# Optimization experiments

Measured on AMD Instinct MI355X. Metric: run time of the kernel, lower is better.

Reference implementation:

```python
import jax, jax.numpy as jnp
import numpy as np

LOG_2PI = np.float32(np.log(2.0 * np.pi))


def _expect(features, labels, pi, mu, sigma):
    # features [N,A], labels [N], pi [C,K], mu [C,K,A], sigma [C,K,A,A]
    d = features.shape[1]
    K = pi.shape[1]
    pi_n = pi[labels]                      # [N,K]
    mu_n = mu[labels]                      # [N,K,A]
    # invert / slogdet per (class, cluster) once, then gather (same math as
    # inverting the per-sample gathered sigma, but C*K inversions not N*K)
    inv_sigma = jnp.linalg.inv(sigma)[labels]          # [N,K,A,A]
    logdet = jnp.linalg.slogdet(sigma)[1][labels]      # [N,K]
    diff = features[:, None, :] - mu_n                 # [N,K,A]
    dist = jnp.einsum('nkd,nkde,nke->nk', diff, inv_sigma, diff)
    # NOTE: sign of the d*log(2pi) term follows the original code verbatim
    log_p = -(dist - d * LOG_2PI + logdet) / 2.0       # [N,K]
    onehot = jax.nn.one_hot(jnp.argmax(log_p, axis=1), K, dtype=features.dtype)
    q_un = onehot * pi_n
    return q_un / (q_un.sum(axis=1, keepdims=True) + 1e-30)


def setup_inputs() -> dict:
    key = jax.random.key(0)
    ks = jax.random.split(key, 6)
    N, C, K, A = 2048, 100, 4, 128
    features = jax.random.normal(ks[0], (N, A), dtype=jnp.float32)
    weight = jax.random.normal(ks[1], (C, A), dtype=jnp.float32) * 0.05
    bias = jnp.zeros((C,), dtype=jnp.float32)
    pi = jax.random.uniform(ks[2], (C, K), dtype=jnp.float32) + 0.1
    pi = pi / pi.sum(axis=1, keepdims=True)
    mu = jax.random.normal(ks[3], (C, K, A), dtype=jnp.float32)
    # SPD covariance stack: B B^T / A + I
    B = jax.random.normal(ks[4], (C, K, A, A), dtype=jnp.float32) * 0.3
    sigma = jnp.einsum('ckij,cklj->ckil', B, B) / A + jnp.eye(A, dtype=jnp.float32)
    labels = jax.random.randint(ks[5], (N,), 0, C, dtype=jnp.int64)
    ratio = jnp.float32(0.5)
    return {"features": features, "weight": weight, "bias": bias,
            "pi": pi, "mu": mu, "sigma": sigma, "labels": labels,
            "ratio": ratio}


def reference(features, weight, bias, pi, mu, sigma, labels, ratio):
    N, A = features.shape
    C, K = pi.shape
    y = features @ weight.T + bias                     # fc(features)  [N,C]
    # NxW_ij - NxW_kj : row j of W minus row label[n] of W, per sample
    diff_w = weight[None, :, :] - weight[labels][:, None, :]   # [N,C,A]
    q = _expect(features, labels, pi, mu, sigma)               # [N,K]
    onehot_q = jax.nn.one_hot(jnp.argmax(q, axis=1), K, dtype=features.dtype)
    CV = jnp.einsum('nkde,nk->nde', sigma[labels], onehot_q)   # [N,A,A]
    # diagonal of ratio * (dW) CV (dW)^T, computed without the [N,C,C] matrix
    sigma2 = ratio * jnp.einsum('nca,nab,ncb->nc', diff_w, CV, diff_w)
    aug = y + 0.5 * sigma2                                     # [N,C]
    logp = jax.nn.log_softmax(aug, axis=-1)
    loss = -jnp.mean(jnp.take_along_axis(logp, labels[:, None], axis=1))
    return (loss, y)
```

## Files before the change

### kernel.cpp

```cpp
#include <hip/hip_runtime.h>
#include <hip/hip_bf16.h>
#include <cmath>

#define N_S    2048
#define C_CLS  100
#define K_CL   4
#define A_DIM  128
#define LDSROW 132
#define NB     16
#define MAXPER 96
#define WTPAD  101
#define SPB    8

__device__ __forceinline__ float gj_invert_lds(
    float* As, float* Rbuf, float* DinvS, int tid)
{
    const int lane = tid & 63;
    const int wv   = tid >> 6;
    float logdet = 0.0f;

    for (int t = 0; t < 8; ++t) {
        const int p0 = NB * t;

        if (wv == 0) {
            const int r = lane >> 2, cg = lane & 3;
            float4 dv = *(const float4*)&As[(p0 + r) * LDSROW + p0 + 4 * cg];
            #pragma unroll
            for (int p = 0; p < NB; ++p) {
                const int sel = p & 3, pr4 = p >> 2;
                float te = (sel == 0) ? dv.x : (sel == 1) ? dv.y : (sel == 2) ? dv.z : dv.w;
                float piv = __shfl(te, (p << 2) | pr4, 64);
                float ip  = 1.0f / piv;
                logdet += __logf(piv);
                const int rowsrc = (p << 2) | cg;
                float4 prs;
                prs.x = __shfl(dv.x, rowsrc, 64) * ip;
                prs.y = __shfl(dv.y, rowsrc, 64) * ip;
                prs.z = __shfl(dv.z, rowsrc, 64) * ip;
                prs.w = __shfl(dv.w, rowsrc, 64) * ip;
                if (cg == pr4) (&prs.x)[sel] = ip;
                float f = __shfl(te, (lane & ~3) | pr4, 64);
                if (r == p) {
                    dv = prs;
                } else {
                    dv.x -= f * prs.x; dv.y -= f * prs.y;
                    dv.z -= f * prs.z; dv.w -= f * prs.w;
                    if (cg == pr4) (&dv.x)[sel] = -f * ip;
                }
            }
            DinvS[r * 17 + 4 * cg + 0] = dv.x;
            DinvS[r * 17 + 4 * cg + 1] = dv.y;
            DinvS[r * 17 + 4 * cg + 2] = dv.z;
            DinvS[r * 17 + 4 * cg + 3] = dv.w;
        }
        __syncthreads();

        {
            const int rr = tid >> 5, j4c = tid & 31;
            float4 o;
            if ((j4c >> 2) == t) {
                const int cg = j4c & 3;
                o.x = DinvS[rr * 17 + 4 * cg + 0];
                o.y = DinvS[rr * 17 + 4 * cg + 1];
                o.z = DinvS[rr * 17 + 4 * cg + 2];
                o.w = DinvS[rr * 17 + 4 * cg + 3];
            } else {
                o.x = 0.f; o.y = 0.f; o.z = 0.f; o.w = 0.f;
                #pragma unroll 4
                for (int k = 0; k < NB; ++k) {
                    const float a = DinvS[rr * 17 + k];
                    const float4 s4 = *(const float4*)&As[(p0 + k) * LDSROW + 4 * j4c];
                    o.x += a * s4.x; o.y += a * s4.y; o.z += a * s4.z; o.w += a * s4.w;
                }
            }
            *(float4*)&Rbuf[rr * A_DIM + 4 * j4c] = o;
        }
        __syncthreads();

        if (tid < 448) {
            const int rgi = tid >> 4;
            const int cp  = tid & 15;
            const int rga = (rgi < 4 * t) ? rgi : rgi + 4;
            const int row0 = 4 * rga;
            const int c0 = 8 * cp, c1 = 8 * cp + 4;
            const bool pcol = ((cp >> 1) == t);
            float4 a00, a01, a10, a11, a20, a21, a30, a31;
            if (pcol) {
                a00 = a01 = a10 = a11 = a20 = a21 = a30 = a31 = (float4){0, 0, 0, 0};
            } else {
                a00 = *(const float4*)&As[(row0 + 0) * LDSROW + c0];
                a01 = *(const float4*)&As[(row0 + 0) * LDSROW + c1];
                a10 = *(const float4*)&As[(row0 + 1) * LDSROW + c0];
                a11 = *(const float4*)&As[(row0 + 1) * LDSROW + c1];
                a20 = *(const float4*)&As[(row0 + 2) * LDSROW + c0];
                a21 = *(const float4*)&As[(row0 + 2) * LDSROW + c1];
                a30 = *(const float4*)&As[(row0 + 3) * LDSROW + c0];
                a31 = *(const float4*)&As[(row0 + 3) * LDSROW + c1];
            }
            #pragma unroll 4
            for (int k = 0; k < NB; ++k) {
                const float4 r0 = *(const float4*)&Rbuf[k * A_DIM + c0];
                const float4 r1 = *(const float4*)&Rbuf[k * A_DIM + c1];
                const float f0 = As[(row0 + 0) * LDSROW + p0 + k];
                const float f1 = As[(row0 + 1) * LDSROW + p0 + k];
                const float f2 = As[(row0 + 2) * LDSROW + p0 + k];
                const float f3 = As[(row0 + 3) * LDSROW + p0 + k];
                a00.x -= f0 * r0.x; a00.y -= f0 * r0.y; a00.z -= f0 * r0.z; a00.w -= f0 * r0.w;
                a01.x -= f0 * r1.x; a01.y -= f0 * r1.y; a01.z -= f0 * r1.z; a01.w -= f0 * r1.w;
                a10.x -= f1 * r0.x; a10.y -= f1 * r0.y; a10.z -= f1 * r0.z; a10.w -= f1 * r0.w;
                a11.x -= f1 * r1.x; a11.y -= f1 * r1.y; a11.z -= f1 * r1.z; a11.w -= f1 * r1.w;
                a20.x -= f2 * r0.x; a20.y -= f2 * r0.y; a20.z -= f2 * r0.z; a20.w -= f2 * r0.w;
                a21.x -= f2 * r1.x; a21.y -= f2 * r1.y; a21.z -= f2 * r1.z; a21.w -= f2 * r1.w;
                a30.x -= f3 * r0.x; a30.y -= f3 * r0.y; a30.z -= f3 * r0.z; a30.w -= f3 * r0.w;
                a31.x -= f3 * r1.x; a31.y -= f3 * r1.y; a31.z -= f3 * r1.z; a31.w -= f3 * r1.w;
            }
            *(float4*)&As[(row0 + 0) * LDSROW + c0] = a00;
            *(float4*)&As[(row0 + 0) * LDSROW + c1] = a01;
            *(float4*)&As[(row0 + 1) * LDSROW + c0] = a10;
            *(float4*)&As[(row0 + 1) * LDSROW + c1] = a11;
            *(float4*)&As[(row0 + 2) * LDSROW + c0] = a20;
            *(float4*)&As[(row0 + 2) * LDSROW + c1] = a21;
            *(float4*)&As[(row0 + 3) * LDSROW + c0] = a30;
            *(float4*)&As[(row0 + 3) * LDSROW + c1] = a31;
        }
        {
            const int rr = tid >> 5, j4c = tid & 31;
            *(float4*)&As[(p0 + rr) * LDSROW + 4 * j4c] =
                *(const float4*)&Rbuf[rr * A_DIM + 4 * j4c];
        }
        __syncthreads();
    }
    return logdet;
}

template<int R>
__device__ __forceinline__ void gsweep(
    const float* __restrict__ As, const float* __restrict__ weight,
    int c0, int lane, float wc0, float wc1, int bid,
    float* __restrict__ gdiag, float* __restrict__ gcol)
{
    const int c0u = __builtin_amdgcn_readfirstlane(c0);
    const float* wr[R];
    #pragma unroll
    for (int r = 0; r < R; ++r) {
        int c = c0u + r; c = (c < C_CLS) ? c : (C_CLS - 1);
        wr[r] = weight + (size_t)c * A_DIM;
    }
    float h0[R], h1[R];
    #pragma unroll
    for (int r = 0; r < R; ++r) { h0[r] = 0.f; h1[r] = 0.f; }
    #pragma unroll 2
    for (int i = 0; i < A_DIM; ++i) {
        const float s0 = As[i * LDSROW + lane];
        const float s1 = As[i * LDSROW + 64 + lane];
        #pragma unroll
        for (int r = 0; r < R; ++r) {
            const float b = wr[r][i];
            h0[r] += b * s0; h1[r] += b * s1;
        }
    }
    #pragma unroll
    for (int r = 0; r < R; ++r) {
        const int c = c0 + r;
        if (c < C_CLS) {
            float pd = h0[r] * weight[c * A_DIM + lane]
                     + h1[r] * weight[c * A_DIM + 64 + lane];
            float pc = h0[r] * wc0 + h1[r] * wc1;
            #pragma unroll
            for (int off = 32; off; off >>= 1) {
                pd += __shfl_xor(pd, off, 64);
                pc += __shfl_xor(pc, off, 64);
            }
            if (lane == 0) {
                gdiag[bid * C_CLS + c] = pd;
                gcol [bid * C_CLS + c] = pc;
            }
        }
    }
}

__global__ __launch_bounds__(512, 2) void k_fused(
    const float* __restrict__ sigma, const float* __restrict__ mu,
    const float* __restrict__ features, const int* __restrict__ labels,
    const float* __restrict__ weight, float* __restrict__ score,
    float* __restrict__ gdiag, float* __restrict__ gcol)
{
    __shared__ __align__(16) float As[A_DIM * LDSROW];
    __shared__ __align__(16) float Scratch[NB * A_DIM + 16*33];
    __shared__ float DinvS[NB * 17];
    __shared__ float ldS;
    __shared__ int idxL[MAXPER];
    __shared__ int cntA;

    const int tid  = threadIdx.x;
    const int bid  = blockIdx.x;
    const int cl   = bid >> 2;
    const int lane = tid & 63;
    const int wv   = tid >> 6;

    if (tid == 0) cntA = 0;

    const float4* src = (const float4*)(sigma + (size_t)bid * A_DIM * A_DIM);
    for (int e4 = tid; e4 < A_DIM * 32; e4 += 512) {
        int i = e4 >> 5, j4 = e4 & 31;
        *(float4*)&As[i * LDSROW + 4 * j4] = src[e4];
    }
    __syncthreads();

    for (int n = tid; n < N_S; n += 512) {
        if (labels[n] == cl) {
            int s = atomicAdd(&cntA, 1);
            if (s < MAXPER) idxL[s] = n;
        }
    }
    {
        const float wc0 = weight[cl * A_DIM + lane];
        const float wc1 = weight[cl * A_DIM + 64 + lane];
        gsweep<13>(As, weight, wv * 13, lane, wc0, wc1, bid, gdiag, gcol);
    }
    __syncthreads();

    float logdet = gj_invert_lds(As, Scratch, DinvS, tid);
    if (tid == 0) ldS = logdet;
    __syncthreads();
    const float ld = ldS;
    const int cnt = min(cntA, MAXPER);

    float* Dbuf = Scratch;
    float* Par  = Scratch + NB * A_DIM;
    const int s16 = tid >> 5;
    const int fc  = tid & 31;
    const float4 muv = ((const float4*)mu)[bid * 32 + fc];

    for (int c0 = 0; c0 < cnt; c0 += 16) {
        const int m = cnt - c0 < 16 ? cnt - c0 : 16;
        if (s16 < m) {
            const int n = idxL[c0 + s16];
            const float4 f = ((const float4*)features)[n * 32 + fc];
            float4 dv;
            dv.x = f.x - muv.x; dv.y = f.y - muv.y;
            dv.z = f.z - muv.z; dv.w = f.w - muv.w;
            *(float4*)&Dbuf[s16 * A_DIM + 4 * fc] = dv;
        }
        __syncthreads();
        if (s16 < m) {
            float4 p = {0.f, 0.f, 0.f, 0.f};
            #pragma unroll 4
            for (int i = 0; i < A_DIM; ++i) {
                const float  d = Dbuf[s16 * A_DIM + i];
                const float4 a = *(const float4*)&As[i * LDSROW + 4 * fc];
                p.x += d * a.x; p.y += d * a.y; p.z += d * a.z; p.w += d * a.w;
            }
            const float4 dj = *(const float4*)&Dbuf[s16 * A_DIM + 4 * fc];
            Par[s16 * 33 + fc] = p.x * dj.x + p.y * dj.y + p.z * dj.z + p.w * dj.w;
        }
        __syncthreads();
        if (tid < m) {
            const int n = idxL[c0 + tid];
            float q = 0.f;
            #pragma unroll
            for (int j = 0; j < 32; ++j) q += Par[tid * 33 + j];
            score[n * K_CL + (bid & 3)] = q + ld;
        }
        __syncthreads();
    }
}

__global__ __launch_bounds__(256) void k_out(
    const float* __restrict__ features, const float* __restrict__ weight,
    const float* __restrict__ bias, const int* __restrict__ labels,
    const float* __restrict__ score, const float* __restrict__ gdiag,
    const float* __restrict__ gcol, const float* __restrict__ ratio_p,
    float* __restrict__ y, float* __restrict__ loss)
{
    __shared__ float Wt[A_DIM * WTPAD];
    __shared__ float bs[C_CLS];
    __shared__ __align__(16) float xs[2][A_DIM];
    __shared__ float red[2][2], red2[2][2], acl_s[2], lsum;

    const int tid  = threadIdx.x;
    const int half = tid >> 7;
    const int t    = tid & 127;

    for (int u = tid; u < C_CLS * 32; u += 256) {
        const int c = u >> 5, j4 = u & 31;
        const float4 w = ((const float4*)weight)[u];
        Wt[(4 * j4 + 0) * WTPAD + c] = w.x;
        Wt[(4 * j4 + 1) * WTPAD + c] = w.y;
        Wt[(4 * j4 + 2) * WTPAD + c] = w.z;
        Wt[(4 * j4 + 3) * WTPAD + c] = w.w;
    }
    if (tid < C_CLS) bs[tid] = bias[tid];
    if (tid == 0) lsum = 0.f;
    __syncthreads();

    const float ratio = *ratio_p;

    for (int p = 0; p < SPB; p += 2) {
        const int n = blockIdx.x * SPB + p + half;
        if (t < 32) ((float4*)xs[half])[t] = ((const float4*)features)[n * 32 + t];
        __syncthreads();

        const int cl = labels[n];
        float s0 = score[n * 4 + 0], s1 = score[n * 4 + 1];
        float s2 = score[n * 4 + 2], s3 = score[n * 4 + 3];
        int ks = 0; float bsv = s0;
        if (s1 < bsv) { bsv = s1; ks = 1; }
        if (s2 < bsv) { bsv = s2; ks = 2; }
        if (s3 < bsv) { bsv = s3; ks = 3; }

        const int base = (cl * 4 + ks) * C_CLS;
        const float gll = gdiag[base + cl];
        float aug = -INFINITY;
        if (t < C_CLS) {
            float acc = bs[t];
            #pragma unroll 4
            for (int j = 0; j < A_DIM; ++j)
                acc += xs[half][j] * Wt[j * WTPAD + t];
            y[(size_t)n * C_CLS + t] = acc;
            aug = acc + 0.5f * ratio * (gdiag[base + t] - 2.0f * gcol[base + t] + gll);
        }

        float m = aug;
        #pragma unroll
        for (int off = 32; off; off >>= 1) m = fmaxf(m, __shfl_xor(m, off, 64));
        if ((t & 63) == 0) red[half][t >> 6] = m;
        __syncthreads();
        m = fmaxf(red[half][0], red[half][1]);

        float e = (t < C_CLS) ? expf(aug - m) : 0.0f;
        #pragma unroll
        for (int off = 32; off; off >>= 1) e += __shfl_xor(e, off, 64);
        if ((t & 63) == 0) red2[half][t >> 6] = e;
        if (t == cl) acl_s[half] = aug;
        __syncthreads();

        if (t == 0) {
            float lp = acl_s[half] - m - logf(red2[half][0] + red2[half][1]);
            atomicAdd(&lsum, -lp);
        }
        __syncthreads();
    }
    if (tid == 0) atomicAdd(loss, lsum * (1.0f / (float)N_S));
}

extern "C" void kernel_launch(void* const* d_in, const int* in_sizes, int n_in,
                              void* d_out, int out_size, void* d_ws, size_t ws_size,
                              hipStream_t stream) {
    const float* features = (const float*)d_in[0];
    const float* weight   = (const float*)d_in[1];
    const float* bias     = (const float*)d_in[2];
    const float* mu       = (const float*)d_in[4];
    const float* sigma    = (const float*)d_in[5];
    const int*   labels   = (const int*)d_in[6];
    const float* ratio    = (const float*)d_in[7];

    float* out   = (float*)d_out;
    float* yout  = out + 1;
    float* score = (float*)d_ws;
    float* gdiag = score + N_S * K_CL;
    float* gcol  = gdiag + C_CLS * K_CL * C_CLS;

    hipMemsetAsync(d_out, 0, sizeof(float), stream);

    k_fused<<<dim3(C_CLS * K_CL), dim3(512), 0, stream>>>(sigma, mu, features, labels,
                                                          weight, score, gdiag, gcol);
    k_out  <<<dim3(N_S / SPB),    dim3(256), 0, stream>>>(features, weight, bias, labels,
                                                          score, gdiag, gcol, ratio, yout, out);
}
```

Before: 210.5 us.

## Stage weight rows in LDS for the sigma-weight sweep and remap GJ update columns

The per-wave sweep that read 13 weight rows straight from global memory is replaced by a loop over 7 chunks. Each chunk loads 16 weight rows into LDS scratch and each wave computes 2 classes from there. This swaps scattered global loads for LDS reads but adds 14 block barriers and recomputes the padded rows. The Gauss-Jordan trailing update also changes its column mapping from 8 contiguous columns to two 4-wide halves 64 apart, to change the LDS bank access pattern.

Result: slower. 221.5 us (+5.2%).

```diff
diff --git a/kernel.cpp b/kernel.cpp
--- a/kernel.cpp
+++ b/kernel.cpp
@@ -82,19 +82,24 @@
             const int cp  = tid & 15;
             const int rga = (rgi < 4 * t) ? rgi : rgi + 4;
             const int row0 = 4 * rga;
-            const int c0 = 8 * cp, c1 = 8 * cp + 4;
-            const bool pcol = ((cp >> 1) == t);
+            const int c0 = 4 * cp, c1 = 64 + 4 * cp;
+            const bool pc0 = ((cp >> 2) == t);
+            const bool pc1 = (((cp >> 2) + 4) == t);
             float4 a00, a01, a10, a11, a20, a21, a30, a31;
-            if (pcol) {
-                a00 = a01 = a10 = a11 = a20 = a21 = a30 = a31 = (float4){0, 0, 0, 0};
+            if (pc0) {
+                a00 = a10 = a20 = a30 = (float4){0, 0, 0, 0};
             } else {
                 a00 = *(const float4*)&As[(row0 + 0) * LDSROW + c0];
+                a10 = *(const float4*)&As[(row0 + 1) * LDSROW + c0];
+                a20 = *(const float4*)&As[(row0 + 2) * LDSROW + c0];
+                a30 = *(const float4*)&As[(row0 + 3) * LDSROW + c0];
+            }
+            if (pc1) {
+                a01 = a11 = a21 = a31 = (float4){0, 0, 0, 0};
+            } else {
                 a01 = *(const float4*)&As[(row0 + 0) * LDSROW + c1];
-                a10 = *(const float4*)&As[(row0 + 1) * LDSROW + c0];
                 a11 = *(const float4*)&As[(row0 + 1) * LDSROW + c1];
-                a20 = *(const float4*)&As[(row0 + 2) * LDSROW + c0];
                 a21 = *(const float4*)&As[(row0 + 2) * LDSROW + c1];
-                a30 = *(const float4*)&As[(row0 + 3) * LDSROW + c0];
                 a31 = *(const float4*)&As[(row0 + 3) * LDSROW + c1];
             }
             #pragma unroll 4
@@ -133,52 +138,6 @@
     return logdet;
 }
 
-template<int R>
-__device__ __forceinline__ void gsweep(
-    const float* __restrict__ As, const float* __restrict__ weight,
-    int c0, int lane, float wc0, float wc1, int bid,
-    float* __restrict__ gdiag, float* __restrict__ gcol)
-{
-    const int c0u = __builtin_amdgcn_readfirstlane(c0);
-    const float* wr[R];
-    #pragma unroll
-    for (int r = 0; r < R; ++r) {
-        int c = c0u + r; c = (c < C_CLS) ? c : (C_CLS - 1);
-        wr[r] = weight + (size_t)c * A_DIM;
-    }
-    float h0[R], h1[R];
-    #pragma unroll
-    for (int r = 0; r < R; ++r) { h0[r] = 0.f; h1[r] = 0.f; }
-    #pragma unroll 2
-    for (int i = 0; i < A_DIM; ++i) {
-        const float s0 = As[i * LDSROW + lane];
-        const float s1 = As[i * LDSROW + 64 + lane];
-        #pragma unroll
-        for (int r = 0; r < R; ++r) {
-            const float b = wr[r][i];
-            h0[r] += b * s0; h1[r] += b * s1;
-        }
-    }
-    #pragma unroll
-    for (int r = 0; r < R; ++r) {
-        const int c = c0 + r;
-        if (c < C_CLS) {
-            float pd = h0[r] * weight[c * A_DIM + lane]
-                     + h1[r] * weight[c * A_DIM + 64 + lane];
-            float pc = h0[r] * wc0 + h1[r] * wc1;
-            #pragma unroll
-            for (int off = 32; off; off >>= 1) {
-                pd += __shfl_xor(pd, off, 64);
-                pc += __shfl_xor(pc, off, 64);
-            }
-            if (lane == 0) {
-                gdiag[bid * C_CLS + c] = pd;
-                gcol [bid * C_CLS + c] = pc;
-            }
-        }
-    }
-}
-
 __global__ __launch_bounds__(512, 2) void k_fused(
     const float* __restrict__ sigma, const float* __restrict__ mu,
     const float* __restrict__ features, const int* __restrict__ labels,
@@ -213,10 +172,61 @@
             if (s < MAXPER) idxL[s] = n;
         }
     }
+
     {
         const float wc0 = weight[cl * A_DIM + lane];
         const float wc1 = weight[cl * A_DIM + 64 + lane];
-        gsweep<13>(As, weight, wv * 13, lane, wc0, wc1, bid, gdiag, gcol);
+        const int cL0 = wv * 2, cL1 = wv * 2 + 1;
+        for (int ch = 0; ch < 7; ++ch) {
+            const int cbase = ch * 16;
+            __syncthreads();
+            {
+                const int r = tid >> 5, j4 = tid & 31;
+                const int crow = min(cbase + r, C_CLS - 1);
+                *(float4*)&Scratch[r * A_DIM + 4 * j4] =
+                    ((const float4*)weight)[crow * 32 + j4];
+            }
+            __syncthreads();
+            float h00 = 0.f, h10 = 0.f, h01 = 0.f, h11 = 0.f;
+            #pragma unroll 2
+            for (int i = 0; i < A_DIM; ++i) {
+                const float s0 = As[i * LDSROW + lane];
+                const float s1 = As[i * LDSROW + 64 + lane];
+                const float b0 = Scratch[cL0 * A_DIM + i];
+                const float b1 = Scratch[cL1 * A_DIM + i];
+                h00 += b0 * s0; h10 += b0 * s1;
+                h01 += b1 * s0; h11 += b1 * s1;
+            }
+            const int ca = cbase + cL0, cb = cbase + cL1;
+            if (ca < C_CLS) {
+                float pd = h00 * Scratch[cL0 * A_DIM + lane]
+                         + h10 * Scratch[cL0 * A_DIM + 64 + lane];
+                float pc = h00 * wc0 + h10 * wc1;
+                #pragma unroll
+                for (int off = 32; off; off >>= 1) {
+                    pd += __shfl_xor(pd, off, 64);
+                    pc += __shfl_xor(pc, off, 64);
+                }
+                if (lane == 0) {
+                    gdiag[bid * C_CLS + ca] = pd;
+                    gcol [bid * C_CLS + ca] = pc;
+                }
+            }
+            if (cb < C_CLS) {
+                float pd = h01 * Scratch[cL1 * A_DIM + lane]
+                         + h11 * Scratch[cL1 * A_DIM + 64 + lane];
+                float pc = h01 * wc0 + h11 * wc1;
+                #pragma unroll
+                for (int off = 32; off; off >>= 1) {
+                    pd += __shfl_xor(pd, off, 64);
+                    pc += __shfl_xor(pc, off, 64);
+                }
+                if (lane == 0) {
+                    gdiag[bid * C_CLS + cb] = pd;
+                    gcol [bid * C_CLS + cb] = pc;
+                }
+            }
+        }
     }
     __syncthreads();
 
```
